# Optimization experiments

Hardware: AMD Instinct MI355X
Metric: run time of the kernel (lower is better)

## Reference

```python
import jax, jax.numpy as jnp
import numpy as np

K = 16          # neighbors per center (init arg K)
EPS = 1e-5      # layernorm epsilon


def _dcconv(pos, ch, W, b, n_in, n_out, resnet_in=None, Wres=None, bres=None):
    """KNN-gathered distance-contained conv.
    pos: [B, n_in, 3], ch: [B, n_in, Cin], W: [Cout, K, Cin].
    Selects n_out strided centers, gathers K nearest neighbors, convolves.
    """
    stride = n_in // n_out
    idx = jnp.arange(n_out) * stride                      # static center indices
    cpos = pos[:, idx]                                    # [B, n_out, 3]
    # squared pairwise distances centers -> all points: [B, n_out, n_in]
    d2 = jnp.sum((cpos[:, :, None, :] - pos[:, None, :, :]) ** 2, axis=-1)
    _, knn = jax.lax.top_k(-d2, K)                        # [B, n_out, K]
    gathered = jax.vmap(lambda c, i: c[i])(ch, knn)       # [B, n_out, K, Cin]
    out = jnp.einsum('bnkc,okc->bno', gathered, W) + b    # [B, n_out, Cout]
    if resnet_in is None:
        res = ch[:, idx] @ Wres + bres                    # project skip to Cout
    else:
        res = resnet_in[:, idx]                           # downsample carried skip
    return cpos, out, res


def _layernorm(x, g, b):
    mu = jnp.mean(x, axis=-1, keepdims=True)
    var = jnp.var(x, axis=-1, keepdims=True)
    return (x - mu) * jax.lax.rsqrt(var + EPS) * g + b


def setup_inputs() -> dict:
    key = jax.random.key(0)
    ks = jax.random.split(key, 8)
    B, N, Cin, Cout = 2, 8192, 64, 128
    s1 = (2.0 / (K * Cin)) ** 0.5
    s2 = (2.0 / (K * Cout)) ** 0.5
    return {
        'position_matrix': jax.random.normal(ks[0], (B, N, 3), jnp.float32),
        'channel_matrix': jax.random.normal(ks[1], (B, N, Cin), jnp.float32),
        'W1': jax.random.normal(ks[2], (Cout, K, Cin), jnp.float32) * s1,
        'b1': jnp.full((Cout,), 0.01, jnp.float32),
        'Wres': jax.random.normal(ks[3], (Cin, Cout), jnp.float32) * (2.0 / Cin) ** 0.5,
        'bres': jnp.full((Cout,), 0.01, jnp.float32),
        'W2': jax.random.normal(ks[4], (Cout, K, Cout), jnp.float32) * s2,
        'b2': jnp.full((Cout,), 0.01, jnp.float32),
        'g1': jnp.ones((Cout,), jnp.float32),
        'be1': jnp.full((Cout,), 0.01, jnp.float32),
        'g2': jnp.ones((Cout,), jnp.float32),
        'be2': jnp.full((Cout,), 0.01, jnp.float32),
        'n0': 8192, 'n1': 4096, 'n2': 2048,
    }


def reference(position_matrix, channel_matrix, W1, b1, Wres, bres, W2, b2,
              g1, be1, g2, be2, n0, n1, n2):
    pos, ch, res = _dcconv(position_matrix, channel_matrix, W1, b1, n0, n1,
                           None, Wres, bres)
    ch = jax.nn.silu(_layernorm(ch, g1, be1))   # dropout=identity (eval)
    pos, ch, res = _dcconv(pos, ch, W2, b2, n1, n2, resnet_in=res)
    ch = jax.nn.silu(_layernorm(ch, g2, be2))   # dropout=identity (eval)
    ch = ch + res                               # residual add
    return pos, ch
```

## Files before the change

### kernel.cpp

```cpp
#include <hip/hip_runtime.h>
#include <cstdint>
#include <cstddef>

using u16 = unsigned short;
using u32 = unsigned int;
using u64 = unsigned long long;

typedef short bf16x8 __attribute__((ext_vector_type(8)));
typedef float f32x4 __attribute__((ext_vector_type(4)));

constexpr int N0 = 8192;
constexpr int N1 = 4096;
constexpr int N2 = 2048;
constexpr int COUT = 128;
constexpr int KNB = 16;

__device__ __forceinline__ float bf2f(u16 v) { return __uint_as_float(((u32)v) << 16); }
__device__ __forceinline__ u16 f2bf(float f) {
    u32 u = __float_as_uint(f);
    return (u16)((u + 0x7fffu + ((u >> 16) & 1u)) >> 16);
}
__device__ __forceinline__ void cvt8(const float* __restrict__ src, u16* __restrict__ dst, int e) {
    float t0[8];
    *(float4*)t0 = *(const float4*)(src + e);
    *(float4*)(t0 + 4) = *(const float4*)(src + e + 4);
    u16 o[8];
#pragma unroll
    for (int q = 0; q < 8; ++q) o[q] = f2bf(t0[q]);
    *(uint4*)(dst + e) = *(uint4*)o;
}

__device__ __forceinline__ float dist2s(float cx, float cy, float cz,
                                        float px, float py, float pz) {
#pragma clang fp contract(off)
    float dx = cx - px;
    float dy = cy - py;
    float dz = cz - pz;
    float s = dx * dx;
    s = s + dy * dy;
    s = s + dz * dz;
    return s;
}

template <int CTRL>
__device__ __forceinline__ u64 dpp64(u64 v) {
    int lo = (int)(u32)v, hi = (int)(u32)(v >> 32);
    int plo = __builtin_amdgcn_update_dpp(0, lo, CTRL, 0xF, 0xF, true);
    int phi = __builtin_amdgcn_update_dpp(0, hi, CTRL, 0xF, 0xF, true);
    return (((u64)(u32)phi) << 32) | (u32)plo;
}
__device__ __forceinline__ u64 dpp_prev_u64(u64 v) { return dpp64<0x111>(v); }

__device__ __forceinline__ u32 rdlane(u32 v, int l) {
    return (u32)__builtin_amdgcn_readlane((int)v, l);
}

template <int PSTRIDE>
__device__ __forceinline__ void knn_scan(const float* __restrict__ P,
                                         int c0row, int c1row, int cnt,
                                         int lane, u64& rk0, u64& rk1) {
    const float* c0p = P + (size_t)c0row * PSTRIDE;
    const float* c1p = P + (size_t)c1row * PSTRIDE;
    float c0x = c0p[0], c0y = c0p[1], c0z = c0p[2];
    float c1x = c1p[0], c1y = c1p[1], c1z = c1p[2];

    u64 key0, key1;
    {
        const float* pp = P + (size_t)lane * PSTRIDE;
        float px = pp[0], py = pp[1], pz = pp[2];
        u64 k0 = (((u64)__float_as_uint(dist2s(c0x, c0y, c0z, px, py, pz))) << 32) | (u32)lane;
        u64 k1 = (((u64)__float_as_uint(dist2s(c1x, c1y, c1z, px, py, pz))) << 32) | (u32)lane;
#pragma unroll
        for (int kk = 2; kk <= 64; kk <<= 1)
#pragma unroll
            for (int jj = kk >> 1; jj > 0; jj >>= 1) {
                u64 o0, o1;
                if (jj == 1)      { o0 = dpp64<0xB1>(k0);  o1 = dpp64<0xB1>(k1); }
                else if (jj == 2) { o0 = dpp64<0x4E>(k0);  o1 = dpp64<0x4E>(k1); }
                else if (jj == 8) { o0 = dpp64<0x128>(k0); o1 = dpp64<0x128>(k1); }
                else              { o0 = __shfl_xor(k0, jj, 64); o1 = __shfl_xor(k1, jj, 64); }
                bool keepmin = (((lane & jj) == 0) == ((lane & kk) == 0));
                k0 = keepmin ? ((o0 < k0) ? o0 : k0) : ((o0 > k0) ? o0 : k0);
                k1 = keepmin ? ((o1 < k1) ? o1 : k1) : ((o1 > k1) ? o1 : k1);
            }
        key0 = k0; key1 = k1;
    }
    u32 cut0 = rdlane((u32)(key0 >> 32), 15);
    u32 cut1 = rdlane((u32)(key1 >> 32), 15);

    {
        const float* pp = P + (size_t)(64 + lane) * PSTRIDE;
        float px = pp[0], py = pp[1], pz = pp[2];
        u32 d0 = __float_as_uint(dist2s(c0x, c0y, c0z, px, py, pz));
        u32 d1 = __float_as_uint(dist2s(c1x, c1y, c1z, px, py, pz));
        u64 ball0 = __ballot(d0 <= cut0);
        u64 ball1 = __ballot(d1 <= cut1);
        while (ball0 | ball1) {
            if (ball0) {
                int src = __ffsll((unsigned long long)ball0) - 1;
                ball0 &= ball0 - 1;
                u64 nk = (((u64)rdlane(d0, src)) << 32) | (u32)(64 + src);
                u64 prev = dpp_prev_u64(key0);
                key0 = (nk < key0) ? ((nk < prev) ? prev : nk) : key0;
            }
            if (ball1) {
                int src = __ffsll((unsigned long long)ball1) - 1;
                ball1 &= ball1 - 1;
                u64 nk = (((u64)rdlane(d1, src)) << 32) | (u32)(64 + src);
                u64 prev = dpp_prev_u64(key1);
                key1 = (nk < key1) ? ((nk < prev) ? prev : nk) : key1;
            }
        }
        cut0 = rdlane((u32)(key0 >> 32), 15);
        cut1 = rdlane((u32)(key1 >> 32), 15);
    }

    constexpr int STEPF = 128 * PSTRIDE;
    int nstep = (cnt - 128) >> 7;
    const float* cur = P + (size_t)(128 + 2 * lane) * PSTRIDE;
    float ax = cur[0], ay = cur[1], az = cur[2];
    float bx = cur[PSTRIDE], by = cur[PSTRIDE + 1], bz = cur[PSTRIDE + 2];
    for (int s = 0; s < nstep; ++s) {
        float cax = ax, cay = ay, caz = az, cbx = bx, cby = by, cbz = bz;
        cur += STEPF;
        if (s + 1 < nstep) {
            ax = cur[0]; ay = cur[1]; az = cur[2];
            bx = cur[PSTRIDE]; by = cur[PSTRIDE + 1]; bz = cur[PSTRIDE + 2];
        }
        int sb = 128 + (s << 7);
        u32 da0 = __float_as_uint(dist2s(c0x, c0y, c0z, cax, cay, caz));
        u32 da1 = __float_as_uint(dist2s(c1x, c1y, c1z, cax, cay, caz));
        u32 db0 = __float_as_uint(dist2s(c0x, c0y, c0z, cbx, cby, cbz));
        u32 db1 = __float_as_uint(dist2s(c1x, c1y, c1z, cbx, cby, cbz));
        u64 ba0 = __ballot(da0 <= cut0);
        u64 bb0 = __ballot(db0 <= cut0);
        u64 ba1 = __ballot(da1 <= cut1);
        u64 bb1 = __ballot(db1 <= cut1);
        while (ba0 | bb0 | ba1 | bb1) {
            if (ba0) {
                int src = __ffsll((unsigned long long)ba0) - 1;
                ba0 &= ba0 - 1;
                u64 nk = (((u64)rdlane(da0, src)) << 32) | (u32)(sb + 2 * src);
                u64 prev = dpp_prev_u64(key0);
                key0 = (nk < key0) ? ((nk < prev) ? prev : nk) : key0;
            }
            if (ba1) {
                int src = __ffsll((unsigned long long)ba1) - 1;
                ba1 &= ba1 - 1;
                u64 nk = (((u64)rdlane(da1, src)) << 32) | (u32)(sb + 2 * src);
                u64 prev = dpp_prev_u64(key1);
                key1 = (nk < key1) ? ((nk < prev) ? prev : nk) : key1;
            }
            if (bb0) {
                int src = __ffsll((unsigned long long)bb0) - 1;
                bb0 &= bb0 - 1;
                u64 nk = (((u64)rdlane(db0, src)) << 32) | (u32)(sb + 2 * src + 1);
                u64 prev = dpp_prev_u64(key0);
                key0 = (nk < key0) ? ((nk < prev) ? prev : nk) : key0;
            }
            if (bb1) {
                int src = __ffsll((unsigned long long)bb1) - 1;
                bb1 &= bb1 - 1;
                u64 nk = (((u64)rdlane(db1, src)) << 32) | (u32)(sb + 2 * src + 1);
                u64 prev = dpp_prev_u64(key1);
                key1 = (nk < key1) ? ((nk < prev) ? prev : nk) : key1;
            }
        }
        cut0 = rdlane((u32)(key0 >> 32), 15);
        cut1 = rdlane((u32)(key1 >> 32), 15);
    }
    rk0 = key0; rk1 = key1;
}

__global__ __launch_bounds__(256)
void knn_prep_kernel(const float* __restrict__ pos0, const float* __restrict__ ch0,
                     const float* __restrict__ W1, const float* __restrict__ W2,
                     const float* __restrict__ Wres,
                     int* __restrict__ knn1,
                     u16* __restrict__ ch0b, u16* __restrict__ W1b,
                     u16* __restrict__ W2b, u16* __restrict__ Wresb,
                     float* __restrict__ pos_out) {
    int blk = blockIdx.x, tid = threadIdx.x;
    int w = tid >> 6, lane = tid & 63;
    if (blk < 1024) {
        int wave = blk * 4 + w;
        int batch = wave >> 11, pj = wave & 2047;
        const float* P = pos0 + (size_t)batch * N0 * 3;
        u64 key0, key1;
        knn_scan<3>(P, 4 * pj, 4 * pj + 2, N0, lane, key0, key1);
        if (lane < 16) {
            knn1[((size_t)(batch * N1 + 2 * pj)) * KNB + lane] = (int)(u32)key0;
            knn1[((size_t)(batch * N1 + 2 * pj + 1)) * KNB + lane] = (int)(u32)key1;
        }
    } else if (blk < 1536) {
        cvt8(ch0, ch0b, ((blk - 1024) * 256 + tid) * 8);
    } else if (blk < 1600) {
        cvt8(W1, W1b, ((blk - 1536) * 256 + tid) * 8);
    } else if (blk < 1728) {
        cvt8(W2, W2b, ((blk - 1600) * 256 + tid) * 8);
    } else if (blk < 1760) {
        int t = (blk - 1728) * 256 + tid;
        int o = t >> 6, c = t & 63;
        Wresb[o * 64 + c] = f2bf(Wres[(size_t)c * COUT + o]);
    } else {
        int t = (blk - 1760) * 256 + tid;
        int b = t >> 11, r = t & 2047;
        const float* s = pos0 + ((size_t)(b * N0 + r * 4)) * 3;
        float* d = pos_out + ((size_t)(b * N2 + r)) * 3;
        d[0] = s[0]; d[1] = s[1]; d[2] = s[2];
    }
}

__global__ __launch_bounds__(256)
void conv1_knn2_kernel(const u16* __restrict__ ch0b, const int* __restrict__ knn1,
                       const u16* __restrict__ W1b, const u16* __restrict__ Wresb,
                       const float* __restrict__ b1, const float* __restrict__ bres,
                       const float* __restrict__ g1, const float* __restrict__ be1,
                       u16* __restrict__ ch1b, u16* __restrict__ res1b,
                       const float* __restrict__ pos0, int* __restrict__ knn2) {
    __shared__ u16 As[16][72];
    __shared__ u16 Ws[128][72];
    __shared__ int knnr[16][16];
    __shared__ float red[16][4][2];
    __shared__ float cb[128], cg[128], cbe[128], cbr[128];

    int blk = blockIdx.x, tid = threadIdx.x;

    if (blk < 512) {
        int w = tid >> 6, lane = tid & 63;
        int wave = blk * 4 + w;
        int batch = wave >> 10, pj = wave & 1023;
        const float* P = pos0 + (size_t)batch * N0 * 3;
        u64 key0, key1;
        knn_scan<6>(P, 4 * pj, 4 * pj + 2, N1, lane, key0, key1);
        if (lane < 16) {
            knn2[((size_t)(batch * N2 + 2 * pj)) * KNB + lane] = (int)(u32)key0;
            knn2[((size_t)(batch * N2 + 2 * pj + 1)) * KNB + lane] = (int)(u32)key1;
        }
        return;
    }

    int cblk = blk - 512;
    int b = cblk >> 8, g = cblk & 255;
    int jbase = g * 16;

    if (tid < 128) { cb[tid] = b1[tid]; cg[tid] = g1[tid]; cbe[tid] = be1[tid]; cbr[tid] = bres[tid]; }
    {
        int r = tid >> 4, k = tid & 15;
        knnr[r][k] = knn1[((size_t)(b * N1 + jbase + r)) * KNB + k];
    }
    __syncthreads();

    int w = tid >> 6, lane = tid & 63, quad = lane >> 4, l15 = lane & 15;
    int wcol = w * 32;
    int ar = tid >> 4, ap = tid & 15;
    int wn = tid >> 1, wh = tid & 1;

    f32x4 acc[2] = {{0,0,0,0},{0,0,0,0}};
    f32x4 racc[2] = {{0,0,0,0},{0,0,0,0}};

    uint2 aR = *((const uint2*)(ch0b + ((size_t)(b * N0 + knnr[ar][0])) * 64) + ap);
    uint4 wR[4];
    {
        const uint4* s4 = (const uint4*)(W1b + (size_t)wn * 1024 + wh * 32);
        wR[0] = s4[0]; wR[1] = s4[1]; wR[2] = s4[2]; wR[3] = s4[3];
    }
    for (int kn = 0; kn < 17; ++kn) {
        *(uint2*)&As[ar][ap * 4] = aR;
        uint4* d4 = (uint4*)&Ws[wn][wh * 32];
        d4[0] = wR[0]; d4[1] = wR[1]; d4[2] = wR[2]; d4[3] = wR[3];
        __syncthreads();
        if (kn < 16) {
            int nidx = (kn < 15) ? knnr[ar][kn + 1] : 2 * (jbase + ar);
            aR = *((const uint2*)(ch0b + ((size_t)(b * N0 + nidx)) * 64) + ap);
            const uint4* s4 = (kn < 15)
                ? (const uint4*)(W1b + (size_t)wn * 1024 + (kn + 1) * 64 + wh * 32)
                : (const uint4*)(Wresb + (size_t)wn * 64 + wh * 32);
            wR[0] = s4[0]; wR[1] = s4[1]; wR[2] = s4[2]; wR[3] = s4[3];
        }
        if (kn < 16) {
#pragma unroll
            for (int ks = 0; ks < 2; ++ks) {
                bf16x8 af = *(const bf16x8*)&As[l15][ks * 32 + quad * 8];
#pragma unroll
                for (int nt = 0; nt < 2; ++nt) {
                    bf16x8 bfr = *(const bf16x8*)&Ws[wcol + nt * 16 + l15][ks * 32 + quad * 8];
                    acc[nt] = __builtin_amdgcn_mfma_f32_16x16x32_bf16(af, bfr, acc[nt], 0, 0, 0);
                }
            }
        } else {
#pragma unroll
            for (int ks = 0; ks < 2; ++ks) {
                bf16x8 af = *(const bf16x8*)&As[l15][ks * 32 + quad * 8];
#pragma unroll
                for (int nt = 0; nt < 2; ++nt) {
                    bf16x8 bfr = *(const bf16x8*)&Ws[wcol + nt * 16 + l15][ks * 32 + quad * 8];
                    racc[nt] = __builtin_amdgcn_mfma_f32_16x16x32_bf16(af, bfr, racc[nt], 0, 0, 0);
                }
            }
        }
        __syncthreads();
    }

    float x[2][4], s[4] = {0,0,0,0}, ss[4] = {0,0,0,0};
#pragma unroll
    for (int reg = 0; reg < 4; ++reg)
#pragma unroll
        for (int nt = 0; nt < 2; ++nt) {
            int col = wcol + nt * 16 + l15;
            float v = acc[nt][reg] + cb[col];
            x[nt][reg] = v;
            s[reg] += v; ss[reg] += v * v;
        }
#pragma unroll
    for (int m = 1; m < 16; m <<= 1)
#pragma unroll
        for (int reg = 0; reg < 4; ++reg) {
            s[reg] += __shfl_xor(s[reg], m, 64);
            ss[reg] += __shfl_xor(ss[reg], m, 64);
        }
    if (l15 == 0) {
#pragma unroll
        for (int reg = 0; reg < 4; ++reg) {
            red[quad * 4 + reg][w][0] = s[reg];
            red[quad * 4 + reg][w][1] = ss[reg];
        }
    }
    __syncthreads();
    float mu[4], rs[4];
#pragma unroll
    for (int reg = 0; reg < 4; ++reg) {
        int row = quad * 4 + reg;
        float S = red[row][0][0] + red[row][1][0] + red[row][2][0] + red[row][3][0];
        float SS = red[row][0][1] + red[row][1][1] + red[row][2][1] + red[row][3][1];
        mu[reg] = S * (1.f / 128.f);
        float var = fmaxf(SS * (1.f / 128.f) - mu[reg] * mu[reg], 0.f);
        rs[reg] = 1.f / sqrtf(var + 1e-5f);
    }
#pragma unroll
    for (int nt = 0; nt < 2; ++nt)
#pragma unroll
        for (int reg = 0; reg < 4; ++reg) {
            int col = wcol + nt * 16 + l15;
            int row = quad * 4 + reg;
            size_t off = ((size_t)(b * N1 + jbase + row)) * COUT + col;
            float y = (x[nt][reg] - mu[reg]) * rs[reg] * cg[col] + cbe[col];
            ch1b[off] = f2bf(y / (1.f + __expf(-y)));
            res1b[off] = f2bf(racc[nt][reg] + cbr[col]);
        }
}

__global__ __launch_bounds__(512)
void conv2_kernel(const u16* __restrict__ ch1b, const int* __restrict__ knn2,
                  const u16* __restrict__ W2b, const float* __restrict__ b2,
                  const float* __restrict__ g2, const float* __restrict__ be2,
                  const u16* __restrict__ res1b, float* __restrict__ ch_out) {
    __shared__ u16 As[16][136];
    __shared__ u16 Ws[128][136];
    __shared__ int knnr[16][16];
    __shared__ float red[16][8][2];
    __shared__ float cb[128], cg[128], cbe[128];

    int tid = threadIdx.x;
    int b = blockIdx.x >> 7, g = blockIdx.x & 127;
    int ibase = g * 16;

    if (tid < 128) { cb[tid] = b2[tid]; cg[tid] = g2[tid]; cbe[tid] = be2[tid]; }
    if (tid < 256) {
        int r = tid >> 4, k = tid & 15;
        knnr[r][k] = knn2[((size_t)(b * N2 + ibase + r)) * KNB + k];
    }
    __syncthreads();

    int w = tid >> 6, lane = tid & 63, quad = lane >> 4, l15 = lane & 15;
    int wcol = w * 16;
    int ar = tid >> 5, ap = tid & 31;
    int wn = tid >> 2, wq = tid & 3;

    f32x4 acc = {0, 0, 0, 0};

    uint2 aR = *((const uint2*)(ch1b + ((size_t)(b * N1 + knnr[ar][0])) * COUT) + ap);
    uint4 wR[4];
    {
        const uint4* s4 = (const uint4*)(W2b + (size_t)wn * 2048 + wq * 32);
        wR[0] = s4[0]; wR[1] = s4[1]; wR[2] = s4[2]; wR[3] = s4[3];
    }
    for (int kn = 0; kn < 16; ++kn) {
        *(uint2*)&As[ar][ap * 4] = aR;
        uint4* d4 = (uint4*)&Ws[wn][wq * 32];
        d4[0] = wR[0]; d4[1] = wR[1]; d4[2] = wR[2]; d4[3] = wR[3];
        __syncthreads();
        if (kn < 15) {
            aR = *((const uint2*)(ch1b + ((size_t)(b * N1 + knnr[ar][kn + 1])) * COUT) + ap);
            const uint4* s4 = (const uint4*)(W2b + (size_t)wn * 2048 + (kn + 1) * 128 + wq * 32);
            wR[0] = s4[0]; wR[1] = s4[1]; wR[2] = s4[2]; wR[3] = s4[3];
        }
#pragma unroll
        for (int ks = 0; ks < 4; ++ks) {
            bf16x8 af = *(const bf16x8*)&As[l15][ks * 32 + quad * 8];
            bf16x8 bfr = *(const bf16x8*)&Ws[wcol + l15][ks * 32 + quad * 8];
            acc = __builtin_amdgcn_mfma_f32_16x16x32_bf16(af, bfr, acc, 0, 0, 0);
        }
        __syncthreads();
    }

    float x[4], s[4], ss[4];
#pragma unroll
    for (int reg = 0; reg < 4; ++reg) {
        int col = wcol + l15;
        float v = acc[reg] + cb[col];
        x[reg] = v; s[reg] = v; ss[reg] = v * v;
    }
#pragma unroll
    for (int m = 1; m < 16; m <<= 1)
#pragma unroll
        for (int reg = 0; reg < 4; ++reg) {
            s[reg] += __shfl_xor(s[reg], m, 64);
            ss[reg] += __shfl_xor(ss[reg], m, 64);
        }
    if (l15 == 0) {
#pragma unroll
        for (int reg = 0; reg < 4; ++reg) {
            red[quad * 4 + reg][w][0] = s[reg];
            red[quad * 4 + reg][w][1] = ss[reg];
        }
    }
    __syncthreads();
#pragma unroll
    for (int reg = 0; reg < 4; ++reg) {
        int row = quad * 4 + reg;
        float S = 0.f, SS = 0.f;
#pragma unroll
        for (int t = 0; t < 8; ++t) { S += red[row][t][0]; SS += red[row][t][1]; }
        float mu = S * (1.f / 128.f);
        float var = fmaxf(SS * (1.f / 128.f) - mu * mu, 0.f);
        float rs = 1.f / sqrtf(var + 1e-5f);
        int col = wcol + l15;
        int i = ibase + row;
        float y = (x[reg] - mu) * rs * cg[col] + cbe[col];
        float sl = y / (1.f + __expf(-y));
        float rv = bf2f(res1b[((size_t)(b * N1 + 2 * i)) * COUT + col]);
        ch_out[((size_t)(b * N2 + i)) * COUT + col] = sl + rv;
    }
}

extern "C" void kernel_launch(void* const* d_in, const int* in_sizes, int n_in,
                              void* d_out, int out_size, void* d_ws, size_t ws_size,
                              hipStream_t stream) {
    const float* pos0 = (const float*)d_in[0];
    const float* ch0  = (const float*)d_in[1];
    const float* W1   = (const float*)d_in[2];
    const float* b1   = (const float*)d_in[3];
    const float* Wres = (const float*)d_in[4];
    const float* bres = (const float*)d_in[5];
    const float* W2   = (const float*)d_in[6];
    const float* b2   = (const float*)d_in[7];
    const float* g1   = (const float*)d_in[8];
    const float* be1  = (const float*)d_in[9];
    const float* g2   = (const float*)d_in[10];
    const float* be2  = (const float*)d_in[11];
    float* out = (float*)d_out;

    char* ws = (char*)d_ws;
    int*  knn1  = (int*)(ws);
    int*  knn2  = (int*)(ws + 524288);
    u16*  ch0b  = (u16*)(ws + 786432);
    u16*  W1b   = (u16*)(ws + 2883584);
    u16*  W2b   = (u16*)(ws + 3145728);
    u16*  Wresb = (u16*)(ws + 3670016);
    u16*  ch1b  = (u16*)(ws + 3686400);
    u16*  res1b = (u16*)(ws + 5783552);

    float* pos_out = out;
    float* ch_out  = out + 12288;

    knn_prep_kernel<<<1776, 256, 0, stream>>>(pos0, ch0, W1, W2, Wres,
                                              knn1, ch0b, W1b, W2b, Wresb, pos_out);
    conv1_knn2_kernel<<<1024, 256, 0, stream>>>(ch0b, knn1, W1b, Wresb, b1, bres, g1, be1,
                                                ch1b, res1b, pos0, knn2);
    conv2_kernel<<<256, 512, 0, stream>>>(ch1b, knn2, W2b, b2, g2, be2, res1b, ch_out);
}
```

Baseline: 221.3 us.

## Replace brute-force KNN scan with x-bucket sort and pruned bidirectional sweep

Adds a sort kernel that bucket-sorts points by the x coordinate (using a monotone float key) for both levels and records each point's rank. The KNN kernels then start from the center's sorted position and sweep outward in 64-point chunks. A side stops once the bucket boundary's x distance exceeds the current 16th-nearest cutoff. This avoids computing distances to all points per center, at the cost of an extra small-grid sort launch, divergent sweeps, and one center per wave instead of two.

```diff
diff --git a/kernel.cpp b/kernel.cpp
--- a/kernel.cpp
+++ b/kernel.cpp
@@ -14,6 +14,11 @@
 constexpr int N2 = 2048;
 constexpr int COUT = 128;
 constexpr int KNB = 16;
+
+constexpr int BSHIFT = 19;
+constexpr int NBUCK = 8192;
+constexpr u32 BMASK = 0xFFF80000u;
+constexpr u32 BINC  = 0x00080000u;
 
 __device__ __forceinline__ float bf2f(u16 v) { return __uint_as_float(((u32)v) << 16); }
 __device__ __forceinline__ u16 f2bf(float f) {
@@ -42,6 +47,13 @@
     return s;
 }
 
+__device__ __forceinline__ u32 monot(u32 u) {
+    return (u & 0x80000000u) ? ~u : (u | 0x80000000u);
+}
+__device__ __forceinline__ float invmono(u32 k) {
+    return (k & 0x80000000u) ? __uint_as_float(k & 0x7FFFFFFFu) : __uint_as_float(~k);
+}
+
 template <int CTRL>
 __device__ __forceinline__ u64 dpp64(u64 v) {
     int lo = (int)(u32)v, hi = (int)(u32)(v >> 32);
@@ -55,155 +67,178 @@
     return (u32)__builtin_amdgcn_readlane((int)v, l);
 }
 
-template <int PSTRIDE>
-__device__ __forceinline__ void knn_scan(const float* __restrict__ P,
-                                         int c0row, int c1row, int cnt,
-                                         int lane, u64& rk0, u64& rk1) {
-    const float* c0p = P + (size_t)c0row * PSTRIDE;
-    const float* c1p = P + (size_t)c1row * PSTRIDE;
-    float c0x = c0p[0], c0y = c0p[1], c0z = c0p[2];
-    float c1x = c1p[0], c1y = c1p[1], c1z = c1p[2];
-
-    u64 key0, key1;
+__global__ __launch_bounds__(256)
+void sort_kernel(const float* __restrict__ pos0,
+                 uint4* __restrict__ sortedA, u32* __restrict__ rankA,
+                 uint4* __restrict__ sortedB, u32* __restrict__ rankB) {
+    __shared__ u32 hist[NBUCK];
+    __shared__ u32 tot[256];
+    int tid = threadIdx.x;
+    int b = blockIdx.x >> 1, lvl = blockIdx.x & 1;
+    int n = lvl ? 4096 : 8192;
+    int pst = lvl ? 6 : 3;
+    const float* P = pos0 + (size_t)b * N0 * 3;
+    uint4* recs = lvl ? (sortedB + (size_t)b * 4096) : (sortedA + (size_t)b * 8192);
+    u32* rank = lvl ? (rankB + (size_t)b * 4096) : (rankA + (size_t)b * 8192);
+
+    for (int i = tid; i < NBUCK; i += 256) hist[i] = 0;
+    __syncthreads();
+    for (int i = tid; i < n; i += 256) {
+        u32 key = monot(__float_as_uint(P[(size_t)i * pst]));
+        atomicAdd(&hist[key >> BSHIFT], 1u);
+    }
+    __syncthreads();
+    u32 vals[32];
+    int base = tid * 32;
+#pragma unroll
+    for (int j = 0; j < 8; ++j) *(uint4*)&vals[j * 4] = *(uint4*)&hist[base + j * 4];
+    u32 run = 0;
+#pragma unroll
+    for (int j = 0; j < 32; ++j) { u32 c = vals[j]; vals[j] = run; run += c; }
+    tot[tid] = run;
+    __syncthreads();
+    for (int off = 1; off < 256; off <<= 1) {
+        u32 v = (tid >= off) ? tot[tid - off] : 0;
+        __syncthreads();
+        tot[tid] += v;
+        __syncthreads();
+    }
+    u32 add = (tid > 0) ? tot[tid - 1] : 0;
+#pragma unroll
+    for (int j = 0; j < 32; ++j) vals[j] += add;
+#pragma unroll
+    for (int j = 0; j < 8; ++j) *(uint4*)&hist[base + j * 4] = *(uint4*)&vals[j * 4];
+    __syncthreads();
+    for (int i = tid; i < n; i += 256) {
+        const float* pp = P + (size_t)i * pst;
+        float x = pp[0], y = pp[1], z = pp[2];
+        u32 key = monot(__float_as_uint(x));
+        u32 slot = atomicAdd(&hist[key >> BSHIFT], 1u);
+        uint4 r;
+        r.x = __float_as_uint(x); r.y = __float_as_uint(y); r.z = __float_as_uint(z);
+        r.w = (u32)i;
+        recs[slot] = r;
+        rank[i] = slot;
+    }
+}
+
+__device__ __forceinline__ u64 knn_sweep(const uint4* __restrict__ recs, int n,
+                                         float cx, float cy, float cz,
+                                         int r0, int lane) {
+    int wb = r0 - 32;
+    if (wb < 0) wb = 0;
+    if (wb > n - 64) wb = n - 64;
+    u64 key;
     {
-        const float* pp = P + (size_t)lane * PSTRIDE;
-        float px = pp[0], py = pp[1], pz = pp[2];
-        u64 k0 = (((u64)__float_as_uint(dist2s(c0x, c0y, c0z, px, py, pz))) << 32) | (u32)lane;
-        u64 k1 = (((u64)__float_as_uint(dist2s(c1x, c1y, c1z, px, py, pz))) << 32) | (u32)lane;
+        uint4 rec = recs[wb + lane];
+        float px = __uint_as_float(rec.x), py = __uint_as_float(rec.y), pz = __uint_as_float(rec.z);
+        u64 k = (((u64)__float_as_uint(dist2s(cx, cy, cz, px, py, pz))) << 32) | rec.w;
 #pragma unroll
         for (int kk = 2; kk <= 64; kk <<= 1)
 #pragma unroll
             for (int jj = kk >> 1; jj > 0; jj >>= 1) {
-                u64 o0, o1;
-                if (jj == 1)      { o0 = dpp64<0xB1>(k0);  o1 = dpp64<0xB1>(k1); }
-                else if (jj == 2) { o0 = dpp64<0x4E>(k0);  o1 = dpp64<0x4E>(k1); }
-                else if (jj == 8) { o0 = dpp64<0x128>(k0); o1 = dpp64<0x128>(k1); }
-                else              { o0 = __shfl_xor(k0, jj, 64); o1 = __shfl_xor(k1, jj, 64); }
+                u64 o;
+                if (jj == 1)      o = dpp64<0xB1>(k);
+                else if (jj == 2) o = dpp64<0x4E>(k);
+                else if (jj == 8) o = dpp64<0x128>(k);
+                else              o = __shfl_xor(k, jj, 64);
                 bool keepmin = (((lane & jj) == 0) == ((lane & kk) == 0));
-                k0 = keepmin ? ((o0 < k0) ? o0 : k0) : ((o0 > k0) ? o0 : k0);
-                k1 = keepmin ? ((o1 < k1) ? o1 : k1) : ((o1 > k1) ? o1 : k1);
+                k = keepmin ? ((o < k) ? o : k) : ((o > k) ? o : k);
             }
-        key0 = k0; key1 = k1;
-    }
-    u32 cut0 = rdlane((u32)(key0 >> 32), 15);
-    u32 cut1 = rdlane((u32)(key1 >> 32), 15);
-
-    {
-        const float* pp = P + (size_t)(64 + lane) * PSTRIDE;
-        float px = pp[0], py = pp[1], pz = pp[2];
-        u32 d0 = __float_as_uint(dist2s(c0x, c0y, c0z, px, py, pz));
-        u32 d1 = __float_as_uint(dist2s(c1x, c1y, c1z, px, py, pz));
-        u64 ball0 = __ballot(d0 <= cut0);
-        u64 ball1 = __ballot(d1 <= cut1);
-        while (ball0 | ball1) {
-            if (ball0) {
-                int src = __ffsll((unsigned long long)ball0) - 1;
-                ball0 &= ball0 - 1;
-                u64 nk = (((u64)rdlane(d0, src)) << 32) | (u32)(64 + src);
-                u64 prev = dpp_prev_u64(key0);
-                key0 = (nk < key0) ? ((nk < prev) ? prev : nk) : key0;
+        key = k;
+    }
+    u32 cut = rdlane((u32)(key >> 32), 15);
+    float cutf = __uint_as_float(cut);
+
+    int R = wb + 64, L = wb - 64;
+    bool rA = (R < n), lA = (L > -64);
+    while (rA || lA) {
+        if (rA) {
+            uint4 rr = recs[min(R + lane, n - 1)];
+            u32 kb = monot(rdlane(rr.x, 0)) & BMASK;
+            float fdx = invmono(kb) - cx;
+            if (fdx > 0.f && fdx * fdx > cutf) {
+                rA = false;
+            } else {
+                float px = __uint_as_float(rr.x), py = __uint_as_float(rr.y), pz = __uint_as_float(rr.z);
+                u32 d = (R + lane < n) ? __float_as_uint(dist2s(cx, cy, cz, px, py, pz))
+                                       : 0xFFFFFFFFu;
+                u64 ball = __ballot(d <= cut);
+                bool any = ball != 0;
+                while (ball) {
+                    int src = __ffsll((unsigned long long)ball) - 1;
+                    ball &= ball - 1;
+                    u64 nk = (((u64)rdlane(d, src)) << 32) | rdlane(rr.w, src);
+                    u64 prev = dpp_prev_u64(key);
+                    key = (nk < key) ? ((nk < prev) ? prev : nk) : key;
+                }
+                if (any) { cut = rdlane((u32)(key >> 32), 15); cutf = __uint_as_float(cut); }
+                R += 64; rA = (R < n);
             }
-            if (ball1) {
-                int src = __ffsll((unsigned long long)ball1) - 1;
-                ball1 &= ball1 - 1;
-                u64 nk = (((u64)rdlane(d1, src)) << 32) | (u32)(64 + src);
-                u64 prev = dpp_prev_u64(key1);
-                key1 = (nk < key1) ? ((nk < prev) ? prev : nk) : key1;
+        }
+        if (lA) {
+            uint4 rr = recs[max(L + lane, 0)];
+            u32 kb = monot(rdlane(rr.x, 63)) & BMASK;
+            bool prune = false;
+            if (kb != BMASK) {
+                float gdx = cx - invmono(kb + BINC);
+                prune = (gdx > 0.f && gdx * gdx > cutf);
             }
-        }
-        cut0 = rdlane((u32)(key0 >> 32), 15);
-        cut1 = rdlane((u32)(key1 >> 32), 15);
-    }
-
-    constexpr int STEPF = 128 * PSTRIDE;
-    int nstep = (cnt - 128) >> 7;
-    const float* cur = P + (size_t)(128 + 2 * lane) * PSTRIDE;
-    float ax = cur[0], ay = cur[1], az = cur[2];
-    float bx = cur[PSTRIDE], by = cur[PSTRIDE + 1], bz = cur[PSTRIDE + 2];
-    for (int s = 0; s < nstep; ++s) {
-        float cax = ax, cay = ay, caz = az, cbx = bx, cby = by, cbz = bz;
-        cur += STEPF;
-        if (s + 1 < nstep) {
-            ax = cur[0]; ay = cur[1]; az = cur[2];
-            bx = cur[PSTRIDE]; by = cur[PSTRIDE + 1]; bz = cur[PSTRIDE + 2];
-        }
-        int sb = 128 + (s << 7);
-        u32 da0 = __float_as_uint(dist2s(c0x, c0y, c0z, cax, cay, caz));
-        u32 da1 = __float_as_uint(dist2s(c1x, c1y, c1z, cax, cay, caz));
-        u32 db0 = __float_as_uint(dist2s(c0x, c0y, c0z, cbx, cby, cbz));
-        u32 db1 = __float_as_uint(dist2s(c1x, c1y, c1z, cbx, cby, cbz));
-        u64 ba0 = __ballot(da0 <= cut0);
-        u64 bb0 = __ballot(db0 <= cut0);
-        u64 ba1 = __ballot(da1 <= cut1);
-        u64 bb1 = __ballot(db1 <= cut1);
-        while (ba0 | bb0 | ba1 | bb1) {
-            if (ba0) {
-                int src = __ffsll((unsigned long long)ba0) - 1;
-                ba0 &= ba0 - 1;
-                u64 nk = (((u64)rdlane(da0, src)) << 32) | (u32)(sb + 2 * src);
-                u64 prev = dpp_prev_u64(key0);
-                key0 = (nk < key0) ? ((nk < prev) ? prev : nk) : key0;
+            if (prune) {
+                lA = false;
+            } else {
+                float px = __uint_as_float(rr.x), py = __uint_as_float(rr.y), pz = __uint_as_float(rr.z);
+                u32 d = (L + lane >= 0) ? __float_as_uint(dist2s(cx, cy, cz, px, py, pz))
+                                        : 0xFFFFFFFFu;
+                u64 ball = __ballot(d <= cut);
+                bool any = ball != 0;
+                while (ball) {
+                    int src = __ffsll((unsigned long long)ball) - 1;
+                    ball &= ball - 1;
+                    u64 nk = (((u64)rdlane(d, src)) << 32) | rdlane(rr.w, src);
+                    u64 prev = dpp_prev_u64(key);
+                    key = (nk < key) ? ((nk < prev) ? prev : nk) : key;
+                }
+                if (any) { cut = rdlane((u32)(key >> 32), 15); cutf = __uint_as_float(cut); }
+                L -= 64; lA = (L > -64);
             }
-            if (ba1) {
-                int src = __ffsll((unsigned long long)ba1) - 1;
-                ba1 &= ba1 - 1;
-                u64 nk = (((u64)rdlane(da1, src)) << 32) | (u32)(sb + 2 * src);
-                u64 prev = dpp_prev_u64(key1);
-                key1 = (nk < key1) ? ((nk < prev) ? prev : nk) : key1;
-            }
-            if (bb0) {
-                int src = __ffsll((unsigned long long)bb0) - 1;
-                bb0 &= bb0 - 1;
-                u64 nk = (((u64)rdlane(db0, src)) << 32) | (u32)(sb + 2 * src + 1);
-                u64 prev = dpp_prev_u64(key0);
-                key0 = (nk < key0) ? ((nk < prev) ? prev : nk) : key0;
-            }
-            if (bb1) {
-                int src = __ffsll((unsigned long long)bb1) - 1;
-                bb1 &= bb1 - 1;
-                u64 nk = (((u64)rdlane(db1, src)) << 32) | (u32)(sb + 2 * src + 1);
-                u64 prev = dpp_prev_u64(key1);
-                key1 = (nk < key1) ? ((nk < prev) ? prev : nk) : key1;
-            }
-        }
-        cut0 = rdlane((u32)(key0 >> 32), 15);
-        cut1 = rdlane((u32)(key1 >> 32), 15);
-    }
-    rk0 = key0; rk1 = key1;
+        }
+    }
+    return key;
 }
 
 __global__ __launch_bounds__(256)
 void knn_prep_kernel(const float* __restrict__ pos0, const float* __restrict__ ch0,
                      const float* __restrict__ W1, const float* __restrict__ W2,
                      const float* __restrict__ Wres,
+                     const uint4* __restrict__ sortedA, const u32* __restrict__ rankA,
                      int* __restrict__ knn1,
                      u16* __restrict__ ch0b, u16* __restrict__ W1b,
                      u16* __restrict__ W2b, u16* __restrict__ Wresb,
                      float* __restrict__ pos_out) {
     int blk = blockIdx.x, tid = threadIdx.x;
     int w = tid >> 6, lane = tid & 63;
-    if (blk < 1024) {
+    if (blk < 2048) {
         int wave = blk * 4 + w;
-        int batch = wave >> 11, pj = wave & 2047;
-        const float* P = pos0 + (size_t)batch * N0 * 3;
-        u64 key0, key1;
-        knn_scan<3>(P, 4 * pj, 4 * pj + 2, N0, lane, key0, key1);
-        if (lane < 16) {
-            knn1[((size_t)(batch * N1 + 2 * pj)) * KNB + lane] = (int)(u32)key0;
-            knn1[((size_t)(batch * N1 + 2 * pj + 1)) * KNB + lane] = (int)(u32)key1;
-        }
-    } else if (blk < 1536) {
-        cvt8(ch0, ch0b, ((blk - 1024) * 256 + tid) * 8);
-    } else if (blk < 1600) {
-        cvt8(W1, W1b, ((blk - 1536) * 256 + tid) * 8);
-    } else if (blk < 1728) {
-        cvt8(W2, W2b, ((blk - 1600) * 256 + tid) * 8);
-    } else if (blk < 1760) {
-        int t = (blk - 1728) * 256 + tid;
+        int batch = wave >> 12, j = wave & 4095;
+        const float* cp = pos0 + ((size_t)(batch * N0 + 2 * j)) * 3;
+        float cx = cp[0], cy = cp[1], cz = cp[2];
+        int r0 = (int)rankA[(size_t)batch * 8192 + 2 * j];
+        u64 key = knn_sweep(sortedA + (size_t)batch * 8192, 8192, cx, cy, cz, r0, lane);
+        if (lane < 16)
+            knn1[((size_t)(batch * N1 + j)) * KNB + lane] = (int)(u32)key;
+    } else if (blk < 2560) {
+        cvt8(ch0, ch0b, ((blk - 2048) * 256 + tid) * 8);
+    } else if (blk < 2624) {
+        cvt8(W1, W1b, ((blk - 2560) * 256 + tid) * 8);
+    } else if (blk < 2752) {
+        cvt8(W2, W2b, ((blk - 2624) * 256 + tid) * 8);
+    } else if (blk < 2784) {
+        int t = (blk - 2752) * 256 + tid;
         int o = t >> 6, c = t & 63;
         Wresb[o * 64 + c] = f2bf(Wres[(size_t)c * COUT + o]);
     } else {
-        int t = (blk - 1760) * 256 + tid;
+        int t = (blk - 2784) * 256 + tid;
         int b = t >> 11, r = t & 2047;
         const float* s = pos0 + ((size_t)(b * N0 + r * 4)) * 3;
         float* d = pos_out + ((size_t)(b * N2 + r)) * 3;
@@ -217,7 +252,9 @@
                        const float* __restrict__ b1, const float* __restrict__ bres,
                        const float* __restrict__ g1, const float* __restrict__ be1,
                        u16* __restrict__ ch1b, u16* __restrict__ res1b,
-                       const float* __restrict__ pos0, int* __restrict__ knn2) {
+                       const float* __restrict__ pos0,
+                       const uint4* __restrict__ sortedB, const u32* __restrict__ rankB,
+                       int* __restrict__ knn2) {
     __shared__ u16 As[16][72];
     __shared__ u16 Ws[128][72];
     __shared__ int knnr[16][16];
@@ -226,21 +263,20 @@
 
     int blk = blockIdx.x, tid = threadIdx.x;
 
-    if (blk < 512) {
+    if (blk >= 512) {
         int w = tid >> 6, lane = tid & 63;
-        int wave = blk * 4 + w;
-        int batch = wave >> 10, pj = wave & 1023;
-        const float* P = pos0 + (size_t)batch * N0 * 3;
-        u64 key0, key1;
-        knn_scan<6>(P, 4 * pj, 4 * pj + 2, N1, lane, key0, key1);
-        if (lane < 16) {
-            knn2[((size_t)(batch * N2 + 2 * pj)) * KNB + lane] = (int)(u32)key0;
-            knn2[((size_t)(batch * N2 + 2 * pj + 1)) * KNB + lane] = (int)(u32)key1;
-        }
+        int wave = (blk - 512) * 4 + w;
+        int batch = wave >> 11, i = wave & 2047;
+        const float* cp = pos0 + ((size_t)(batch * N0 + 4 * i)) * 3;
+        float cx = cp[0], cy = cp[1], cz = cp[2];
+        int r0 = (int)rankB[(size_t)batch * 4096 + 2 * i];
+        u64 key = knn_sweep(sortedB + (size_t)batch * 4096, 4096, cx, cy, cz, r0, lane);
+        if (lane < 16)
+            knn2[((size_t)(batch * N2 + i)) * KNB + lane] = (int)(u32)key;
         return;
     }
 
-    int cblk = blk - 512;
+    int cblk = blk;
     int b = cblk >> 8, g = cblk & 255;
     int jbase = g * 16;
 
@@ -470,13 +506,19 @@
     u16*  Wresb = (u16*)(ws + 3670016);
     u16*  ch1b  = (u16*)(ws + 3686400);
     u16*  res1b = (u16*)(ws + 5783552);
+    uint4* sortedA = (uint4*)(ws + 7880704);
+    uint4* sortedB = (uint4*)(ws + 8142848);
+    u32*  rankA = (u32*)(ws + 8273920);
+    u32*  rankB = (u32*)(ws + 8339456);
 
     float* pos_out = out;
     float* ch_out  = out + 12288;
 
-    knn_prep_kernel<<<1776, 256, 0, stream>>>(pos0, ch0, W1, W2, Wres,
-                                              knn1, ch0b, W1b, W2b, Wresb, pos_out);
-    conv1_knn2_kernel<<<1024, 256, 0, stream>>>(ch0b, knn1, W1b, Wresb, b1, bres, g1, be1,
-                                                ch1b, res1b, pos0, knn2);
+    sort_kernel<<<4, 256, 0, stream>>>(pos0, sortedA, rankA, sortedB, rankB);
+    knn_prep_kernel<<<2800, 256, 0, stream>>>(pos0, ch0, W1, W2, Wres,
+                                              sortedA, rankA, knn1,
+                                              ch0b, W1b, W2b, Wresb, pos_out);
+    conv1_knn2_kernel<<<1536, 256, 0, stream>>>(ch0b, knn1, W1b, Wresb, b1, bres, g1, be1,
+                                                ch1b, res1b, pos0, sortedB, rankB, knn2);
     conv2_kernel<<<256, 512, 0, stream>>>(ch1b, knn2, W2b, b2, g2, be2, res1b, ch_out);
 }
```

After: 251.6 us. 13.7% more time.

## Load conv weights directly into MFMA registers and double-buffer gathered activations

Applied to the files above, without the earlier changes.

Both conv kernels stop staging weight tiles through shared memory. Each lane now loads its MFMA B-operand fragments straight from global memory into registers, with the next neighbour's weights prefetched. The gathered activation tile is double-buffered in shared memory, so one of the two barriers per iteration is removed. In the fused conv1/knn2 kernel the block order is also swapped so the conv blocks come first and the knn scan blocks follow. The changes cut LDS traffic, barriers and shared-memory footprint, at the cost of more redundant global weight reads per wave and higher register pressure.

```diff
diff --git a/kernel.cpp b/kernel.cpp
--- a/kernel.cpp
+++ b/kernel.cpp
@@ -218,17 +218,16 @@
                        const float* __restrict__ g1, const float* __restrict__ be1,
                        u16* __restrict__ ch1b, u16* __restrict__ res1b,
                        const float* __restrict__ pos0, int* __restrict__ knn2) {
-    __shared__ u16 As[16][72];
-    __shared__ u16 Ws[128][72];
+    __shared__ u16 As[2][16][72];
     __shared__ int knnr[16][16];
     __shared__ float red[16][4][2];
     __shared__ float cb[128], cg[128], cbe[128], cbr[128];
 
     int blk = blockIdx.x, tid = threadIdx.x;
 
-    if (blk < 512) {
+    if (blk >= 512) {
         int w = tid >> 6, lane = tid & 63;
-        int wave = blk * 4 + w;
+        int wave = (blk - 512) * 4 + w;
         int batch = wave >> 10, pj = wave & 1023;
         const float* P = pos0 + (size_t)batch * N0 * 3;
         u64 key0, key1;
@@ -240,8 +239,7 @@
         return;
     }
 
-    int cblk = blk - 512;
-    int b = cblk >> 8, g = cblk & 255;
+    int b = blk >> 8, g = blk & 255;
     int jbase = g * 16;
 
     if (tid < 128) { cb[tid] = b1[tid]; cg[tid] = g1[tid]; cbe[tid] = be1[tid]; cbr[tid] = bres[tid]; }
@@ -254,52 +252,56 @@
     int w = tid >> 6, lane = tid & 63, quad = lane >> 4, l15 = lane & 15;
     int wcol = w * 32;
     int ar = tid >> 4, ap = tid & 15;
-    int wn = tid >> 1, wh = tid & 1;
 
     f32x4 acc[2] = {{0,0,0,0},{0,0,0,0}};
     f32x4 racc[2] = {{0,0,0,0},{0,0,0,0}};
 
+    const u16* w0base = W1b + (size_t)(wcol + l15) * 1024 + quad * 8;
+    const u16* w1base = W1b + (size_t)(wcol + 16 + l15) * 1024 + quad * 8;
+
     uint2 aR = *((const uint2*)(ch0b + ((size_t)(b * N0 + knnr[ar][0])) * 64) + ap);
-    uint4 wR[4];
-    {
-        const uint4* s4 = (const uint4*)(W1b + (size_t)wn * 1024 + wh * 32);
-        wR[0] = s4[0]; wR[1] = s4[1]; wR[2] = s4[2]; wR[3] = s4[3];
-    }
+    uint4 wcur[4] = { *(const uint4*)w0base, *(const uint4*)(w0base + 32),
+                      *(const uint4*)w1base, *(const uint4*)(w1base + 32) };
+
+    int pb = 0;
     for (int kn = 0; kn < 17; ++kn) {
-        *(uint2*)&As[ar][ap * 4] = aR;
-        uint4* d4 = (uint4*)&Ws[wn][wh * 32];
-        d4[0] = wR[0]; d4[1] = wR[1]; d4[2] = wR[2]; d4[3] = wR[3];
+        *(uint2*)&As[pb][ar][ap * 4] = aR;
         __syncthreads();
+        uint4 wnxt[4];
         if (kn < 16) {
             int nidx = (kn < 15) ? knnr[ar][kn + 1] : 2 * (jbase + ar);
             aR = *((const uint2*)(ch0b + ((size_t)(b * N0 + nidx)) * 64) + ap);
-            const uint4* s4 = (kn < 15)
-                ? (const uint4*)(W1b + (size_t)wn * 1024 + (kn + 1) * 64 + wh * 32)
-                : (const uint4*)(Wresb + (size_t)wn * 64 + wh * 32);
-            wR[0] = s4[0]; wR[1] = s4[1]; wR[2] = s4[2]; wR[3] = s4[3];
+            if (kn < 15) {
+                const u16* p0 = w0base + (kn + 1) * 64;
+                const u16* p1 = w1base + (kn + 1) * 64;
+                wnxt[0] = *(const uint4*)p0; wnxt[1] = *(const uint4*)(p0 + 32);
+                wnxt[2] = *(const uint4*)p1; wnxt[3] = *(const uint4*)(p1 + 32);
+            } else {
+                const u16* p0 = Wresb + (size_t)(wcol + l15) * 64 + quad * 8;
+                const u16* p1 = Wresb + (size_t)(wcol + 16 + l15) * 64 + quad * 8;
+                wnxt[0] = *(const uint4*)p0; wnxt[1] = *(const uint4*)(p0 + 32);
+                wnxt[2] = *(const uint4*)p1; wnxt[3] = *(const uint4*)(p1 + 32);
+            }
         }
         if (kn < 16) {
 #pragma unroll
             for (int ks = 0; ks < 2; ++ks) {
-                bf16x8 af = *(const bf16x8*)&As[l15][ks * 32 + quad * 8];
-#pragma unroll
-                for (int nt = 0; nt < 2; ++nt) {
-                    bf16x8 bfr = *(const bf16x8*)&Ws[wcol + nt * 16 + l15][ks * 32 + quad * 8];
-                    acc[nt] = __builtin_amdgcn_mfma_f32_16x16x32_bf16(af, bfr, acc[nt], 0, 0, 0);
-                }
+                bf16x8 af = *(const bf16x8*)&As[pb][l15][ks * 32 + quad * 8];
+                acc[0] = __builtin_amdgcn_mfma_f32_16x16x32_bf16(af, *(const bf16x8*)&wcur[ks], acc[0], 0, 0, 0);
+                acc[1] = __builtin_amdgcn_mfma_f32_16x16x32_bf16(af, *(const bf16x8*)&wcur[2 + ks], acc[1], 0, 0, 0);
             }
         } else {
 #pragma unroll
             for (int ks = 0; ks < 2; ++ks) {
-                bf16x8 af = *(const bf16x8*)&As[l15][ks * 32 + quad * 8];
-#pragma unroll
-                for (int nt = 0; nt < 2; ++nt) {
-                    bf16x8 bfr = *(const bf16x8*)&Ws[wcol + nt * 16 + l15][ks * 32 + quad * 8];
-                    racc[nt] = __builtin_amdgcn_mfma_f32_16x16x32_bf16(af, bfr, racc[nt], 0, 0, 0);
-                }
-            }
-        }
-        __syncthreads();
+                bf16x8 af = *(const bf16x8*)&As[pb][l15][ks * 32 + quad * 8];
+                racc[0] = __builtin_amdgcn_mfma_f32_16x16x32_bf16(af, *(const bf16x8*)&wcur[ks], racc[0], 0, 0, 0);
+                racc[1] = __builtin_amdgcn_mfma_f32_16x16x32_bf16(af, *(const bf16x8*)&wcur[2 + ks], racc[1], 0, 0, 0);
+            }
+        }
+        if (kn < 16) {
+            wcur[0] = wnxt[0]; wcur[1] = wnxt[1]; wcur[2] = wnxt[2]; wcur[3] = wnxt[3];
+        }
+        pb ^= 1;
     }
 
     float x[2][4], s[4] = {0,0,0,0}, ss[4] = {0,0,0,0};
@@ -355,8 +357,7 @@
                   const u16* __restrict__ W2b, const float* __restrict__ b2,
                   const float* __restrict__ g2, const float* __restrict__ be2,
                   const u16* __restrict__ res1b, float* __restrict__ ch_out) {
-    __shared__ u16 As[16][136];
-    __shared__ u16 Ws[128][136];
+    __shared__ u16 As[2][16][136];
     __shared__ int knnr[16][16];
     __shared__ float red[16][8][2];
     __shared__ float cb[128], cg[128], cbe[128];
@@ -375,33 +376,35 @@
     int w = tid >> 6, lane = tid & 63, quad = lane >> 4, l15 = lane & 15;
     int wcol = w * 16;
     int ar = tid >> 5, ap = tid & 31;
-    int wn = tid >> 2, wq = tid & 3;
 
     f32x4 acc = {0, 0, 0, 0};
 
+    const u16* wbase = W2b + (size_t)(wcol + l15) * 2048 + quad * 8;
+
     uint2 aR = *((const uint2*)(ch1b + ((size_t)(b * N1 + knnr[ar][0])) * COUT) + ap);
-    uint4 wR[4];
-    {
-        const uint4* s4 = (const uint4*)(W2b + (size_t)wn * 2048 + wq * 32);
-        wR[0] = s4[0]; wR[1] = s4[1]; wR[2] = s4[2]; wR[3] = s4[3];
-    }
+    uint4 wcur[4] = { *(const uint4*)wbase, *(const uint4*)(wbase + 32),
+                      *(const uint4*)(wbase + 64), *(const uint4*)(wbase + 96) };
+
+    int pb = 0;
     for (int kn = 0; kn < 16; ++kn) {
-        *(uint2*)&As[ar][ap * 4] = aR;
-        uint4* d4 = (uint4*)&Ws[wn][wq * 32];
-        d4[0] = wR[0]; d4[1] = wR[1]; d4[2] = wR[2]; d4[3] = wR[3];
+        *(uint2*)&As[pb][ar][ap * 4] = aR;
         __syncthreads();
+        uint4 wnxt[4];
         if (kn < 15) {
             aR = *((const uint2*)(ch1b + ((size_t)(b * N1 + knnr[ar][kn + 1])) * COUT) + ap);
-            const uint4* s4 = (const uint4*)(W2b + (size_t)wn * 2048 + (kn + 1) * 128 + wq * 32);
-            wR[0] = s4[0]; wR[1] = s4[1]; wR[2] = s4[2]; wR[3] = s4[3];
+            const u16* p = wbase + (kn + 1) * 128;
+            wnxt[0] = *(const uint4*)p;        wnxt[1] = *(const uint4*)(p + 32);
+            wnxt[2] = *(const uint4*)(p + 64); wnxt[3] = *(const uint4*)(p + 96);
         }
 #pragma unroll
         for (int ks = 0; ks < 4; ++ks) {
-            bf16x8 af = *(const bf16x8*)&As[l15][ks * 32 + quad * 8];
-            bf16x8 bfr = *(const bf16x8*)&Ws[wcol + l15][ks * 32 + quad * 8];
-            acc = __builtin_amdgcn_mfma_f32_16x16x32_bf16(af, bfr, acc, 0, 0, 0);
-        }
-        __syncthreads();
+            bf16x8 af = *(const bf16x8*)&As[pb][l15][ks * 32 + quad * 8];
+            acc = __builtin_amdgcn_mfma_f32_16x16x32_bf16(af, *(const bf16x8*)&wcur[ks], acc, 0, 0, 0);
+        }
+        if (kn < 15) {
+            wcur[0] = wnxt[0]; wcur[1] = wnxt[1]; wcur[2] = wnxt[2]; wcur[3] = wnxt[3];
+        }
+        pb ^= 1;
     }
 
     float x[4], s[4], ss[4];
```

Result: faster. 189.1 us (-14.6%).
